# Optimization experiments

Measured on AMD Instinct MI355X. Metric: run time of the kernel, lower is better.

The kernel has to match this reference:

```python
import jax, jax.numpy as jnp
import numpy as np

B, S, E, H = 4, 2048, 1024, 16
HD = E // H  # head_dim = 64


def setup_inputs() -> dict:
    key = jax.random.key(0)
    k1, k2, k3, k4 = jax.random.split(key, 4)
    x = jax.random.normal(k1, (B, S, E), dtype=jnp.float32)
    # torch Linear stores weight as (out, in); y = x @ W.T
    w_qkv = jax.random.normal(k2, (3 * E, E), dtype=jnp.float32) * (E ** -0.5)
    w_proj = jax.random.normal(k3, (E, E), dtype=jnp.float32) * (E ** -0.5)
    b_proj = jax.random.normal(k4, (E,), dtype=jnp.float32) * 0.01
    return {"x": x, "w_qkv": w_qkv, "w_proj": w_proj, "b_proj": b_proj}


def reference(x, w_qkv, w_proj, b_proj):
    b, s, e = x.shape
    # fused QKV, then per-head interleaved split (matches view(B,S,H,3*hd).chunk)
    qkv = jnp.einsum('bse,fe->bsf', x, w_qkv).reshape(b, s, H, 3 * HD)
    q, k, v = jnp.split(qkv, 3, axis=-1)  # each (b, s, H, HD)
    scale = HD ** -0.5
    scores = jnp.einsum('bqhd,bkhd->bhqk', q, k) * scale
    causal = jnp.tril(jnp.ones((s, s), dtype=bool))
    scores = jnp.where(causal, scores, jnp.float32(-jnp.inf))
    probs = jax.nn.softmax(scores, axis=-1)
    out = jnp.einsum('bhqk,bkhd->bqhd', probs, v).reshape(b, s, e)
    return jnp.einsum('bse,fe->bsf', out, w_proj) + b_proj
```

## Files before the change

### kernel.cpp

```cpp
#include <hip/hip_runtime.h>

#define Bq   4
#define Sq   2048
#define Eq   1024
#define Hq   16
#define HDq  64
#define Mq   (Bq*Sq)
#define N1q  (3*Eq)
#define Kq   Eq

#define NX4  (Mq*Kq/4)
#define NW4  (N1q*Kq/4)
#define NP4  (Eq*Kq/4)

typedef __bf16 bf16x8 __attribute__((ext_vector_type(8)));
typedef __bf16 bf16x4 __attribute__((ext_vector_type(4)));
typedef float  f32x4  __attribute__((ext_vector_type(4)));
typedef float  f32x16 __attribute__((ext_vector_type(16)));

#define GAS __attribute__((address_space(1)))
#define LAS __attribute__((address_space(3)))

__device__ __forceinline__ void gl2lds16(const void* g, void* l) {
  __builtin_amdgcn_global_load_lds((GAS const void*)g, (LAS void*)l, 16, 0, 0);
}

__device__ __forceinline__ unsigned pack2(float a, float b) {
  union { __bf16 h[2]; unsigned u; } x;
  x.h[0] = (__bf16)a; x.h[1] = (__bf16)b; return x.u;
}

__device__ __forceinline__ void perm32swap(unsigned& a, unsigned& b) {
  asm("v_permlane32_swap_b32 %0, %1" : "+v"(a), "+v"(b));
}

__device__ __forceinline__ float fexp2(float x) {
#if __has_builtin(__builtin_amdgcn_exp2f)
  return __builtin_amdgcn_exp2f(x);
#else
  return exp2f(x);
#endif
}

__global__ __launch_bounds__(256) void cvt_all(const float* __restrict__ x,
                                               const float* __restrict__ wqkv,
                                               const float* __restrict__ wproj,
                                               __bf16* __restrict__ xb,
                                               __bf16* __restrict__ wqkvb,
                                               __bf16* __restrict__ wprojb) {
  int i = blockIdx.x * 256 + threadIdx.x;
  const float* src; __bf16* dst; int j; float sc = 1.0f;
  if (i < NX4) {
    src = x; dst = xb; j = i;
  } else if (i < NX4 + NW4) {
    j = i - NX4; src = wqkv; dst = wqkvb;
    const int row = j >> 8;
    if ((row % 192) < 64) sc = 0.18033688011112042f;
  } else {
    j = i - NX4 - NW4; src = wproj; dst = wprojb;
  }
  float4 v = ((const float4*)src)[j];
  bf16x4 o = { (__bf16)(v.x * sc), (__bf16)(v.y * sc),
               (__bf16)(v.z * sc), (__bf16)(v.w * sc) };
  ((bf16x4*)dst)[j] = o;
}

template <int MODE>
__global__ __launch_bounds__(256) void gemm_bt(const __bf16* __restrict__ A,
                                               const __bf16* __restrict__ Bw,
                                               int N, int K,
                                               __bf16* __restrict__ cbf,
                                               const float* __restrict__ bias,
                                               float* __restrict__ cf32) {
  __shared__ __align__(16) __bf16 As[128 * 64];
  __shared__ __align__(16) __bf16 Bs[128 * 64];
  const int tid  = threadIdx.x;
  const int wave = tid >> 6, lane = tid & 63;
  const int quad = lane >> 4, l15 = lane & 15;
  const int wm = wave & 1, wn = wave >> 1;
  const int bm0 = blockIdx.x * 128;
  const int bn0 = blockIdx.y * 128;

  f32x4 acc[4][4] = {};

  const int ar = tid >> 2;
  const int ac = ((tid & 3) ^ ((tid >> 3) & 3)) * 8;
  const __bf16* Ag0 = A  + (long)(bm0 + ar) * K + ac;
  const __bf16* Bg0 = Bw + (long)(bn0 + ar) * K + ac;
  __bf16* As0 = As + wave * 512;
  __bf16* Bs0 = Bs + wave * 512;

  const int fsw = (l15 >> 1) & 3;
  const int a_rd = (wm * 64 + l15) * 32 + (quad ^ fsw) * 8;
  const int b_rd = (wn * 64 + l15) * 32 + (quad ^ fsw) * 8;

  for (int kc = 0; kc < K; kc += 64) {
    gl2lds16(Ag0 + kc,               As0);
    gl2lds16(Ag0 + 64 * K + kc,      As0 + 2048);
    gl2lds16(Ag0 + kc + 32,          As0 + 4096);
    gl2lds16(Ag0 + 64 * K + kc + 32, As0 + 6144);
    gl2lds16(Bg0 + kc,               Bs0);
    gl2lds16(Bg0 + 64 * K + kc,      Bs0 + 2048);
    gl2lds16(Bg0 + kc + 32,          Bs0 + 4096);
    gl2lds16(Bg0 + 64 * K + kc + 32, Bs0 + 6144);
    __syncthreads();

    bf16x8 af[4], bfr[4];
#pragma unroll
    for (int mt = 0; mt < 4; mt++)
      af[mt] = *(const bf16x8*)&As[a_rd + mt * 512];
#pragma unroll
    for (int nt = 0; nt < 4; nt++)
      bfr[nt] = *(const bf16x8*)&Bs[b_rd + nt * 512];
#pragma unroll
    for (int mt = 0; mt < 4; mt++)
#pragma unroll
      for (int nt = 0; nt < 4; nt++)
        acc[mt][nt] = __builtin_amdgcn_mfma_f32_16x16x32_bf16(af[mt], bfr[nt], acc[mt][nt], 0, 0, 0);

    bf16x8 af1[4], bfr1[4];
#pragma unroll
    for (int mt = 0; mt < 4; mt++)
      af1[mt] = *(const bf16x8*)&As[4096 + a_rd + mt * 512];
#pragma unroll
    for (int nt = 0; nt < 4; nt++)
      bfr1[nt] = *(const bf16x8*)&Bs[4096 + b_rd + nt * 512];
#pragma unroll
    for (int mt = 0; mt < 4; mt++)
#pragma unroll
      for (int nt = 0; nt < 4; nt++)
        acc[mt][nt] = __builtin_amdgcn_mfma_f32_16x16x32_bf16(af1[mt], bfr1[nt], acc[mt][nt], 0, 0, 0);
    __syncthreads();
  }

#pragma unroll
  for (int nt = 0; nt < 4; nt++) {
    const int n = bn0 + wn * 64 + nt * 16 + l15;
    float bv = 0.f;
    if (MODE == 1) bv = bias[n];
#pragma unroll
    for (int mt = 0; mt < 4; mt++) {
      const int mbase = bm0 + wm * 64 + mt * 16 + quad * 4;
#pragma unroll
      for (int r = 0; r < 4; r++) {
        const long m = mbase + r;
        if (MODE == 0) cbf[m * N + n] = (__bf16)acc[mt][nt][r];
        else           cf32[m * N + n] = acc[mt][nt][r] + bv;
      }
    }
  }
}

__global__ __launch_bounds__(256) void transv(const __bf16* __restrict__ qkv,
                                              __bf16* __restrict__ vt) {
  __shared__ __align__(16) __bf16 T[64 * 64];
  const int tid = threadIdx.x, wave = tid >> 6;
  const int bh = blockIdx.x >> 5, st = blockIdx.x & 31;
  const int b = bh >> 4, h = bh & 15;
  const long gbase = (long)(b * Sq + st * 64 + (tid >> 3)) * N1q + h * 192 + 128 + (tid & 7) * 8;
  gl2lds16(qkv + gbase,                  T + wave * 512);
  gl2lds16(qkv + gbase + (long)32 * N1q, T + 2048 + wave * 512);
  __syncthreads();
  const int d = tid >> 2, s4 = (tid & 3) * 16;
  bf16x8 o0, o1;
#pragma unroll
  for (int j = 0; j < 8; j++) o0[j] = T[(s4 + j) * 64 + d];
#pragma unroll
  for (int j = 0; j < 8; j++) o1[j] = T[(s4 + 8 + j) * 64 + d];
  __bf16* dst = vt + (long)(bh * 64 + d) * Sq + st * 64 + s4;
  *(bf16x8*)dst = o0;
  *(bf16x8*)(dst + 8) = o1;
}

__global__ __launch_bounds__(256, 2) void attn_fwd(const __bf16* __restrict__ qkv,
                                                   const __bf16* __restrict__ vt,
                                                   __bf16* __restrict__ aout) {
  __shared__ __align__(16) __bf16 Ks[128 * 64];
  __shared__ __align__(16) __bf16 Vs[64 * 128];

  const int tid = threadIdx.x;
  const int w = tid >> 6, lane = tid & 63;
  const int c = lane & 31, h = lane >> 5;
  const int bi = blockIdx.x;
  const int bh = bi & 63, kk = (bi >> 6) & 3, jr = bi >> 8;
  const int qt = 4 * jr + ((kk + jr) & 3);
  const int b = bh >> 4, head = bh & 15;

  const int krr = lane >> 3, kj = lane & 7;
  const int vrr = lane >> 4, vj = lane & 15;

  const int q_g = qt * 128 + w * 32 + c;

  bf16x8 qf[4];
  const __bf16* qp = qkv + (long)(b * Sq + q_g) * N1q + head * 192 + h * 8;
#pragma unroll
  for (int kc2 = 0; kc2 < 4; kc2++) qf[kc2] = *(const bf16x8*)(qp + kc2 * 16);

  f32x16 oT[2] = {};
  float l_i = 0.f;
  constexpr float MB = 16.0f;

  const int nk = qt + 1;
  for (int kt = 0; kt < nk; kt++) {
#pragma unroll
    for (int i = 0; i < 4; i++) {
      const int row = w * 32 + i * 8 + krr;
      gl2lds16(qkv + (long)(b * Sq + kt * 128 + row) * N1q + head * 192 + 64
                   + (kj ^ (krr & 7)) * 8,
               Ks + (w * 32 + i * 8) * 64);
    }
#pragma unroll
    for (int i = 0; i < 4; i++) {
      const int dr = w * 16 + i * 4 + vrr;
      gl2lds16(vt + (long)(bh * 64 + dr) * Sq + kt * 128 + (vj ^ (dr & 7)) * 8,
               Vs + (w * 16 + i * 4) * 128);
    }
    __syncthreads();

    const bool diag = (kt == qt);
    float s_acc = 0.f;

#pragma unroll
    for (int nf = 0; nf < 4; nf++) {
      f32x16 z = {};
#pragma unroll
      for (int kc2 = 0; kc2 < 4; kc2++) {
        bf16x8 kf = *(const bf16x8*)&Ks[(nf * 32 + c) * 64 + (((kc2 * 2 + h) ^ (c & 7)) * 8)];
        z = __builtin_amdgcn_mfma_f32_32x32x16_bf16(kf, qf[kc2], z, 0, 0, 0);
      }
      if (diag) {
#pragma unroll
        for (int r = 0; r < 16; r++) {
          const int kcol = kt * 128 + nf * 32 + (r & 3) + 8 * (r >> 2) + 4 * h;
          if (kcol > q_g) z[r] = -1e30f;
        }
      }
#pragma unroll
      for (int r = 0; r < 16; r++) {
        float p = fexp2(z[r] - MB);
        z[r] = p; s_acc += p;
      }
#pragma unroll
      for (int sub = 0; sub < 2; sub++) {
        const int kc = nf * 2 + sub, base = 8 * sub;
        unsigned pa0 = pack2(z[base + 0], z[base + 1]);
        unsigned pa1 = pack2(z[base + 2], z[base + 3]);
        unsigned pb0 = pack2(z[base + 4], z[base + 5]);
        unsigned pb1 = pack2(z[base + 6], z[base + 7]);
        perm32swap(pa0, pb0);
        perm32swap(pa1, pb1);
        union { bf16x8 v; unsigned u[4]; } pf;
        pf.u[0] = pa0;
        pf.u[1] = pa1;
        pf.u[2] = pb0;
        pf.u[3] = pb1;
#pragma unroll
        for (int nf2 = 0; nf2 < 2; nf2++) {
          bf16x8 vf = *(const bf16x8*)&Vs[(nf2 * 32 + c) * 128 + (((kc * 2 + h) ^ (c & 7)) * 8)];
          oT[nf2] = __builtin_amdgcn_mfma_f32_32x32x16_bf16(vf, pf.v, oT[nf2], 0, 0, 0);
        }
      }
    }
    l_i += s_acc;
    __syncthreads();
  }

  const float l = l_i + __shfl_xor(l_i, 32);
  const float inv = 1.0f / l;
  const long obase = (long)(b * Sq + q_g) * Eq + head * 64;
#pragma unroll
  for (int nf2 = 0; nf2 < 2; nf2++)
#pragma unroll
    for (int g = 0; g < 4; g++) {
      bf16x4 o;
#pragma unroll
      for (int t = 0; t < 4; t++) o[t] = (__bf16)(oT[nf2][g * 4 + t] * inv);
      *(bf16x4*)(aout + obase + nf2 * 32 + 8 * g + 4 * h) = o;
    }
}

extern "C" void kernel_launch(void* const* d_in, const int* in_sizes, int n_in,
                              void* d_out, int out_size, void* d_ws, size_t ws_size,
                              hipStream_t stream) {
  const float* x      = (const float*)d_in[0];
  const float* w_qkv  = (const float*)d_in[1];
  const float* w_proj = (const float*)d_in[2];
  const float* b_proj = (const float*)d_in[3];
  float* out = (float*)d_out;

  char* w = (char*)d_ws;
  __bf16* xb     = (__bf16*)w; w += (size_t)Mq * Kq * 2;
  __bf16* wqkvb  = (__bf16*)w; w += (size_t)N1q * Kq * 2;
  __bf16* wprojb = (__bf16*)w; w += (size_t)Eq * Kq * 2;
  __bf16* qkvb   = (__bf16*)w; w += (size_t)Mq * N1q * 2;
  __bf16* vtb    = (__bf16*)w; w += (size_t)Bq * Hq * HDq * Sq * 2;
  __bf16* attnb  = (__bf16*)w;

  cvt_all<<<(NX4 + NW4 + NP4) / 256, 256, 0, stream>>>(x, w_qkv, w_proj, xb, wqkvb, wprojb);

  gemm_bt<0><<<dim3(Mq / 128, N1q / 128), 256, 0, stream>>>(xb, wqkvb, N1q, Kq, qkvb, nullptr, nullptr);

  transv<<<Bq * Hq * (Sq / 64), 256, 0, stream>>>(qkvb, vtb);

  attn_fwd<<<16 * 64, 256, 0, stream>>>(qkvb, vtb, attnb);

  gemm_bt<1><<<dim3(Mq / 128, Eq / 128), 256, 0, stream>>>(attnb, wprojb, Eq, Kq, nullptr, b_proj, out);
}
```

Before: 244.0 us.

## Double-buffer K/V tiles in attention to overlap global loads with MFMA compute

Allocates two LDS buffers each for K and V and prefetches the next key tile with global_load_lds while the current tile is computed, with sched_barrier fences keeping the load issue ahead of the compute. This hides global-memory latency behind the MFMA work. It also folds the fixed max-bias subtraction into the score accumulator's initial value, saving one subtraction per score. The cost is double the LDS use (64KB per block), which may limit occupancy under launch_bounds(256,2). Synchronisation relies on a single __syncthreads per stage, so the correctness of the prefetch timing depends on the hardware's wait semantics for LDS DMA loads.

```diff
diff --git a/kernel.cpp b/kernel.cpp
--- a/kernel.cpp
+++ b/kernel.cpp
@@ -175,8 +175,10 @@
 __global__ __launch_bounds__(256, 2) void attn_fwd(const __bf16* __restrict__ qkv,
                                                    const __bf16* __restrict__ vt,
                                                    __bf16* __restrict__ aout) {
-  __shared__ __align__(16) __bf16 Ks[128 * 64];
-  __shared__ __align__(16) __bf16 Vs[64 * 128];
+  __shared__ __align__(16) __bf16 Ks0[128 * 64];
+  __shared__ __align__(16) __bf16 Ks1[128 * 64];
+  __shared__ __align__(16) __bf16 Vs0[64 * 128];
+  __shared__ __align__(16) __bf16 Vs1[64 * 128];
 
   const int tid = threadIdx.x;
   const int w = tid >> 6, lane = tid & 63;
@@ -200,70 +202,94 @@
   float l_i = 0.f;
   constexpr float MB = 16.0f;
 
+#define ATTN_STAGE(KD, VD, kt_) do {                                          \
+    _Pragma("unroll")                                                         \
+    for (int i = 0; i < 4; i++) {                                             \
+      const int row = w * 32 + i * 8 + krr;                                   \
+      gl2lds16(qkv + (long)(b * Sq + (kt_) * 128 + row) * N1q + head * 192    \
+                   + 64 + (kj ^ (krr & 7)) * 8,                               \
+               (KD) + (w * 32 + i * 8) * 64);                                 \
+    }                                                                         \
+    _Pragma("unroll")                                                         \
+    for (int i = 0; i < 4; i++) {                                             \
+      const int dr = w * 16 + i * 4 + vrr;                                    \
+      gl2lds16(vt + (long)(bh * 64 + dr) * Sq + (kt_) * 128                   \
+                  + (vj ^ (dr & 7)) * 8,                                      \
+               (VD) + (w * 16 + i * 4) * 128);                                \
+    }                                                                         \
+  } while (0)
+
+#define ATTN_COMPUTE(KS, VS, kt_) do {                                        \
+    const bool diag = ((kt_) == qt);                                          \
+    float s_acc = 0.f;                                                        \
+    _Pragma("unroll")                                                         \
+    for (int nf = 0; nf < 4; nf++) {                                          \
+      f32x16 z;                                                               \
+      _Pragma("unroll")                                                       \
+      for (int r = 0; r < 16; r++) z[r] = -MB;    \
+      _Pragma("unroll")                                                       \
+      for (int kc2 = 0; kc2 < 4; kc2++) {                                     \
+        bf16x8 kf = *(const bf16x8*)&(KS)[(nf * 32 + c) * 64                  \
+                                          + (((kc2 * 2 + h) ^ (c & 7)) * 8)]; \
+        z = __builtin_amdgcn_mfma_f32_32x32x16_bf16(kf, qf[kc2], z, 0, 0, 0); \
+      }                                                                       \
+      if (diag) {                                                             \
+        _Pragma("unroll")                                                     \
+        for (int r = 0; r < 16; r++) {                                        \
+          const int kcol = (kt_) * 128 + nf * 32 + (r & 3) + 8 * (r >> 2)     \
+                           + 4 * h;                                           \
+          if (kcol > q_g) z[r] = -1e30f;                                      \
+        }                                                                     \
+      }                                                                       \
+      _Pragma("unroll")                                                       \
+      for (int r = 0; r < 16; r++) {                                          \
+        float p = fexp2(z[r]);                                                \
+        z[r] = p; s_acc += p;                                                 \
+      }                                                                       \
+      _Pragma("unroll")                                                       \
+      for (int sub = 0; sub < 2; sub++) {                                     \
+        const int kc = nf * 2 + sub, base = 8 * sub;                          \
+        unsigned pa0 = pack2(z[base + 0], z[base + 1]);                       \
+        unsigned pa1 = pack2(z[base + 2], z[base + 3]);                       \
+        unsigned pb0 = pack2(z[base + 4], z[base + 5]);                       \
+        unsigned pb1 = pack2(z[base + 6], z[base + 7]);                       \
+        perm32swap(pa0, pb0);                                                 \
+        perm32swap(pa1, pb1);                                                 \
+        union { bf16x8 v; unsigned u[4]; } pf;                                \
+        pf.u[0] = pa0; pf.u[1] = pa1; pf.u[2] = pb0; pf.u[3] = pb1;           \
+        _Pragma("unroll")                                                     \
+        for (int nf2 = 0; nf2 < 2; nf2++) {                                   \
+          bf16x8 vf = *(const bf16x8*)&(VS)[(nf2 * 32 + c) * 128              \
+                                            + (((kc * 2 + h) ^ (c & 7)) * 8)];\
+          oT[nf2] = __builtin_amdgcn_mfma_f32_32x32x16_bf16(vf, pf.v,         \
+                                                            oT[nf2], 0, 0, 0);\
+        }                                                                     \
+      }                                                                       \
+    }                                                                         \
+    l_i += s_acc;                                                             \
+  } while (0)
+
   const int nk = qt + 1;
-  for (int kt = 0; kt < nk; kt++) {
-#pragma unroll
-    for (int i = 0; i < 4; i++) {
-      const int row = w * 32 + i * 8 + krr;
-      gl2lds16(qkv + (long)(b * Sq + kt * 128 + row) * N1q + head * 192 + 64
-                   + (kj ^ (krr & 7)) * 8,
-               Ks + (w * 32 + i * 8) * 64);
-    }
-#pragma unroll
-    for (int i = 0; i < 4; i++) {
-      const int dr = w * 16 + i * 4 + vrr;
-      gl2lds16(vt + (long)(bh * 64 + dr) * Sq + kt * 128 + (vj ^ (dr & 7)) * 8,
-               Vs + (w * 16 + i * 4) * 128);
-    }
+  ATTN_STAGE(Ks0, Vs0, 0);
+  __syncthreads();
+
+  int kt = 0;
+  for (; kt + 1 < nk; kt += 2) {
+    ATTN_STAGE(Ks1, Vs1, kt + 1);
+    __builtin_amdgcn_sched_barrier(0);
+    ATTN_COMPUTE(Ks0, Vs0, kt);
     __syncthreads();
 
-    const bool diag = (kt == qt);
-    float s_acc = 0.f;
-
-#pragma unroll
-    for (int nf = 0; nf < 4; nf++) {
-      f32x16 z = {};
-#pragma unroll
-      for (int kc2 = 0; kc2 < 4; kc2++) {
-        bf16x8 kf = *(const bf16x8*)&Ks[(nf * 32 + c) * 64 + (((kc2 * 2 + h) ^ (c & 7)) * 8)];
-        z = __builtin_amdgcn_mfma_f32_32x32x16_bf16(kf, qf[kc2], z, 0, 0, 0);
-      }
-      if (diag) {
-#pragma unroll
-        for (int r = 0; r < 16; r++) {
-          const int kcol = kt * 128 + nf * 32 + (r & 3) + 8 * (r >> 2) + 4 * h;
-          if (kcol > q_g) z[r] = -1e30f;
-        }
-      }
-#pragma unroll
-      for (int r = 0; r < 16; r++) {
-        float p = fexp2(z[r] - MB);
-        z[r] = p; s_acc += p;
-      }
-#pragma unroll
-      for (int sub = 0; sub < 2; sub++) {
-        const int kc = nf * 2 + sub, base = 8 * sub;
-        unsigned pa0 = pack2(z[base + 0], z[base + 1]);
-        unsigned pa1 = pack2(z[base + 2], z[base + 3]);
-        unsigned pb0 = pack2(z[base + 4], z[base + 5]);
-        unsigned pb1 = pack2(z[base + 6], z[base + 7]);
-        perm32swap(pa0, pb0);
-        perm32swap(pa1, pb1);
-        union { bf16x8 v; unsigned u[4]; } pf;
-        pf.u[0] = pa0;
-        pf.u[1] = pa1;
-        pf.u[2] = pb0;
-        pf.u[3] = pb1;
-#pragma unroll
-        for (int nf2 = 0; nf2 < 2; nf2++) {
-          bf16x8 vf = *(const bf16x8*)&Vs[(nf2 * 32 + c) * 128 + (((kc * 2 + h) ^ (c & 7)) * 8)];
-          oT[nf2] = __builtin_amdgcn_mfma_f32_32x32x16_bf16(vf, pf.v, oT[nf2], 0, 0, 0);
-        }
-      }
-    }
-    l_i += s_acc;
+    if (kt + 2 < nk) ATTN_STAGE(Ks0, Vs0, kt + 2);
+    __builtin_amdgcn_sched_barrier(0);
+    ATTN_COMPUTE(Ks1, Vs1, kt + 1);
     __syncthreads();
   }
+  if (kt < nk)
+    ATTN_COMPUTE(Ks0, Vs0, kt);
+
+#undef ATTN_STAGE
+#undef ATTN_COMPUTE
 
   const float l = l_i + __shfl_xor(l_i, 32);
   const float inv = 1.0f / l;
```

Result: slower. 252.3 us (+3.4%).
